# Kernel optimization log

Hardware: AMD Instinct MI355X
Metric: run time of the kernel (lower is better)

Reference implementation:

```python
import jax, jax.numpy as jnp
import numpy as np

K = 20
EPS = 1e-5
SLOPE = 0.2


def knn_idx(x, k):
    # x: (B, C, N) -> neighbor indices (B, N, k) by smallest squared distance
    xx = jnp.sum(x * x, axis=1)                      # (B, N)
    inner = jnp.einsum('bcn,bcm->bnm', x, x)         # (B, N, N)
    neg_dist = 2.0 * inner - xx[:, :, None] - xx[:, None, :]
    return jax.lax.top_k(neg_dist, k)[1]             # (B, N, k)


def bn_lrelu(y, g, b, axes):
    # training-mode BatchNorm (batch stats) + LeakyReLU(0.2); channel = last axis
    m = jnp.mean(y, axis=axes, keepdims=True)
    v = jnp.var(y, axis=axes, keepdims=True)
    y = (y - m) * jax.lax.rsqrt(v + EPS) * g + b
    return jnp.where(y > 0, y, SLOPE * y)


def edge_block(x, W, g, b, k):
    # x: (B, C, N); W: (out, 2C). Returns (B, N, out) = max over k neighbors.
    idx = knn_idx(x, k)                              # (B, N, k)
    xt = jnp.transpose(x, (0, 2, 1))                 # (B, N, C)
    feat = jax.vmap(lambda a, i: a[i])(xt, idx)      # (B, N, k, C) gather
    ctr = jnp.broadcast_to(xt[:, :, None, :], feat.shape)
    e = jnp.concatenate([feat - ctr, ctr], axis=-1)  # (B, N, k, 2C)
    y = jnp.einsum('bnkc,oc->bnko', e, W)            # 1x1 conv
    y = bn_lrelu(y, g, b, (0, 1, 2))
    return jnp.max(y, axis=2)                        # (B, N, out)


def setup_inputs() -> dict:
    key = jax.random.key(0)
    ks = jax.random.split(key, 7)
    feat_dims = [64, 64, 128, 256]
    in_dims = [2 * 3, 2 * 64, 2 * 64, 2 * 128]
    B, N = 8, 1024
    d = {'x': jax.random.normal(ks[0], (B, N, 3), dtype=jnp.float32)}
    for i, (ci, co) in enumerate(zip(in_dims, feat_dims)):
        d[f'W{i}'] = jax.random.normal(ks[i + 1], (co, ci), dtype=jnp.float32) * (1.0 / np.sqrt(ci))
        d[f'g{i}'] = jnp.ones((co,), dtype=jnp.float32)
        d[f'b{i}'] = jnp.zeros((co,), dtype=jnp.float32)
    fuse, emb = sum(feat_dims), 1024
    d['Wf'] = jax.random.normal(ks[5], (emb, fuse), dtype=jnp.float32) * (1.0 / np.sqrt(fuse))
    d['gf'] = jnp.ones((emb,), dtype=jnp.float32)
    d['bf'] = jnp.zeros((emb,), dtype=jnp.float32)
    return d


def reference(x, W0, g0, b0, W1, g1, b1, W2, g2, b2, W3, g3, b3, Wf, gf, bf):
    # x: (B, N, 3) -> (B, N, emb)
    h = jnp.transpose(x, (0, 2, 1))                  # (B, 3, N)
    states = []
    for (W, g, b) in [(W0, g0, b0), (W1, g1, b1), (W2, g2, b2), (W3, g3, b3)]:
        hn = edge_block(h, W, g, b, K)               # (B, N, out)
        states.append(hn)
        h = jnp.transpose(hn, (0, 2, 1))             # (B, out, N)
    fused = jnp.concatenate(states, axis=-1)         # (B, N, 512)
    y = jnp.einsum('bnc,oc->bno', fused, Wf)         # final 1x1 conv
    y = bn_lrelu(y, gf, bf, (0, 1))
    return y
```

## Files before the change

### kernel.cpp

```cpp
#include <hip/hip_runtime.h>
#include <math.h>

#define TILE 64
#define KC 16

typedef __attribute__((ext_vector_type(8))) short short8;
typedef __attribute__((ext_vector_type(4))) float float4v;
typedef const __attribute__((address_space(1))) void* gptr_t;
typedef __attribute__((address_space(3))) void* lptr_t;

#define OFF_DF    0ull
#define OFF_PT    0ull
#define OFF_YMAX  16777216ull
#define OFF_YMIN  25165824ull
#define OFF_YF    0ull
#define OFF_IDX   67108864ull
#define OFF_H     67764224ull
#define OFF_FUSB  76152832ull
#define OFF_WFB   84541440ull
#define OFF_XX    85590016ull
#define OFF_WCAT  85655552ull
#define OFF_STATS 85917696ull
#define OFF_COEF  85942272ull
#define OFF_HHI   85954560ull
#define OFF_HLO   88051712ull

__device__ __forceinline__ unsigned short f2bf(float f) {
  unsigned int u = __float_as_uint(f);
  unsigned int r = (u + 0x7fffu + ((u >> 16) & 1u)) >> 16;
  return (unsigned short)r;
}

__device__ __forceinline__ void gemm_tile_loop(
    const float* __restrict__ A, const float* __restrict__ Bw,
    int K, int lda, int ldb, int rowBase, int colBase,
    float acc[4][4], float* As, float* Bs)
{
  const int tid = threadIdx.x;
  const int tx = tid & 15, ty = tid >> 4;
  for (int k0 = 0; k0 < K; k0 += KC) {
    for (int l = 0; l < 4; ++l) {
      int flat = tid * 4 + l;
      int kk = flat & (KC - 1);
      int row = flat >> 4;
      int gk = k0 + kk;
      float av = 0.f, bv = 0.f;
      if (gk < K) {
        av = A[(size_t)(rowBase + row) * lda + gk];
        bv = Bw[(size_t)(colBase + row) * ldb + gk];
      }
      As[kk * TILE + row] = av;
      Bs[kk * TILE + row] = bv;
    }
    __syncthreads();
#pragma unroll
    for (int kk = 0; kk < KC; ++kk) {
      float a0[4], b0[4];
#pragma unroll
      for (int i = 0; i < 4; ++i) a0[i] = As[kk * TILE + ty * 4 + i];
#pragma unroll
      for (int j = 0; j < 4; ++j) b0[j] = Bs[kk * TILE + tx * 4 + j];
#pragma unroll
      for (int i = 0; i < 4; ++i)
#pragma unroll
        for (int j = 0; j < 4; ++j)
          acc[i][j] = fmaf(a0[i], b0[j], acc[i][j]);
    }
    __syncthreads();
  }
}

__global__ __launch_bounds__(256) void xxf_kernel(const float* __restrict__ H, int C,
                                                  float* __restrict__ xx) {
  int m = blockIdx.x * 256 + threadIdx.x;
  if (m < 8192) {
    float s = 0.f;
    for (int c = 0; c < C; ++c) { float h = H[(size_t)m * C + c]; s = fmaf(h, h, s); }
    xx[m] = s;
  }
}

__global__ __launch_bounds__(256) void split_bf16(const float* __restrict__ H, int C, int l2kp,
                                                  unsigned short* __restrict__ hi,
                                                  unsigned short* __restrict__ lo) {
  int i = blockIdx.x * 256 + threadIdx.x;
  int m = i >> l2kp;
  int c = i & ((1 << l2kp) - 1);
  unsigned short h = 0, l = 0;
  if (c < C) {
    float v = H[(size_t)m * C + c];
    h = f2bf(v);
    float hf = __uint_as_float((unsigned)h << 16);
    l = f2bf(v - hf);
  }
  hi[i] = h;
  lo[i] = l;
}

__global__ __launch_bounds__(256) void dist_mfma(const unsigned short* __restrict__ Hhi,
                                                 const unsigned short* __restrict__ Hlo,
                                                 const float* __restrict__ xx,
                                                 float* __restrict__ Df, int Kp) {
  __shared__ unsigned short Ash[128 * 32], Asl[128 * 32];
  __shared__ unsigned short Bsh[128 * 32], Bsl[128 * 32];
  const int tid = threadIdx.x;
  const int lane = tid & 63;
  const int w = tid >> 6;
  const int wm = w >> 1, wn = w & 1;
  const int bz = blockIdx.z;
  const int rowBase = bz * 1024 + blockIdx.y * 128;
  const int colBase = bz * 1024 + blockIdx.x * 128;
  const int quad = lane >> 4;
  const int l15 = lane & 15;

  float4v acc[4][4] = {};

  for (int k0 = 0; k0 < Kp; k0 += 32) {
#pragma unroll
    for (int q = 0; q < 2; ++q) {
      int ch = (w * 2 + q) * 64 + lane;
      int r = ch >> 2, cp = ch & 3;
      size_t offA = (size_t)(rowBase + r) * Kp + k0 + cp * 8;
      size_t offB = (size_t)(colBase + r) * Kp + k0 + cp * 8;
      int seg = (w * 2 + q) * 512;
      __builtin_amdgcn_global_load_lds((gptr_t)(Hhi + offA), (lptr_t)(Ash + seg), 16, 0, 0);
      __builtin_amdgcn_global_load_lds((gptr_t)(Hlo + offA), (lptr_t)(Asl + seg), 16, 0, 0);
      __builtin_amdgcn_global_load_lds((gptr_t)(Hhi + offB), (lptr_t)(Bsh + seg), 16, 0, 0);
      __builtin_amdgcn_global_load_lds((gptr_t)(Hlo + offB), (lptr_t)(Bsl + seg), 16, 0, 0);
    }
    __syncthreads();
    short8 ah[4], al[4], bh[4], bl[4];
#pragma unroll
    for (int mi = 0; mi < 4; ++mi) {
      int ro = (wm * 64 + mi * 16 + l15) * 32 + quad * 8;
      ah[mi] = *(const short8*)(Ash + ro);
      al[mi] = *(const short8*)(Asl + ro);
    }
#pragma unroll
    for (int ni = 0; ni < 4; ++ni) {
      int ro = (wn * 64 + ni * 16 + l15) * 32 + quad * 8;
      bh[ni] = *(const short8*)(Bsh + ro);
      bl[ni] = *(const short8*)(Bsl + ro);
    }
#pragma unroll
    for (int mi = 0; mi < 4; ++mi)
#pragma unroll
      for (int ni = 0; ni < 4; ++ni) {
        acc[mi][ni] = __builtin_amdgcn_mfma_f32_16x16x32_bf16(ah[mi], bh[ni], acc[mi][ni], 0, 0, 0);
        acc[mi][ni] = __builtin_amdgcn_mfma_f32_16x16x32_bf16(ah[mi], bl[ni], acc[mi][ni], 0, 0, 0);
        acc[mi][ni] = __builtin_amdgcn_mfma_f32_16x16x32_bf16(al[mi], bh[ni], acc[mi][ni], 0, 0, 0);
      }
    __syncthreads();
  }
#pragma unroll
  for (int mi = 0; mi < 4; ++mi)
#pragma unroll
    for (int ni = 0; ni < 4; ++ni)
#pragma unroll
      for (int r = 0; r < 4; ++r) {
        int gm = rowBase + wm * 64 + mi * 16 + quad * 4 + r;
        int gn = blockIdx.x * 128 + wn * 64 + ni * 16 + l15;
        float v = 2.0f * acc[mi][ni][r] - xx[gm] - xx[bz * 1024 + gn];
        Df[(size_t)gm * 1024 + gn] = v;
      }
}

template<int C>
__global__ __launch_bounds__(256) void topk_rerank(const float* __restrict__ Df,
                                                   const float* __restrict__ H,
                                                   int* __restrict__ idx) {
  __shared__ int    candLds[4][64];
  __shared__ double ndLds[4][64];
  __shared__ int    colLds[4][64];
  const int lane = threadIdx.x & 63;
  const int w = threadIdx.x >> 6;
  const int row = blockIdx.x * 4 + w;
  const int b = row >> 10;
  const float* drow = Df + (size_t)row * 1024;

  unsigned s[16];
#pragma unroll
  for (int q = 0; q < 4; ++q) {
    float4v v = *(const float4v*)(drow + 256 * q + 4 * lane);
#pragma unroll
    for (int r = 0; r < 4; ++r) {
      float f = (r == 0) ? v.x : (r == 1) ? v.y : (r == 2) ? v.z : v.w;
      unsigned u = __float_as_uint(f);
      s[q * 4 + r] = (u & 0x80000000u) ? ~u : (u | 0x80000000u);
    }
  }

  unsigned p = 0;
  for (int bit = 31; bit >= 0; --bit) {
    unsigned cand = p | (1u << bit);
    int c = 0;
#pragma unroll
    for (int t = 0; t < 16; ++t)
      c += __popcll(__ballot(s[t] > cand));
    if (c >= 32) {
      p = cand;
      if (c <= 64) break;
    }
  }

  const unsigned long long lt = (1ull << lane) - 1ull;
  int base = 0;
#pragma unroll
  for (int t = 0; t < 16; ++t) {
    unsigned long long m = __ballot(s[t] > p);
    if (s[t] > p) {
      int slot = base + (int)__popcll(m & lt);
      if (slot < 64) candLds[w][slot] = 256 * (t >> 2) + 4 * lane + (t & 3);
    }
    base += (int)__popcll(m);
  }
  int nsel = base > 64 ? 64 : base;

  double nd; int col;
  if (lane < nsel) {
    col = candLds[w][lane];
    const float* xi = H + (size_t)row * C;
    const float* xj = H + (size_t)(b * 1024 + col) * C;
    double ssum = 0.0;
    if (C == 3) {
#pragma unroll
      for (int c = 0; c < 3; ++c) {
        double d = (double)xi[c] - (double)xj[c];
        ssum = fma(d, d, ssum);
      }
    } else {
      for (int c = 0; c < C; c += 4) {
        float4v a = *(const float4v*)(xi + c);
        float4v bb = *(const float4v*)(xj + c);
        double d0 = (double)a.x - (double)bb.x;
        double d1 = (double)a.y - (double)bb.y;
        double d2 = (double)a.z - (double)bb.z;
        double d3 = (double)a.w - (double)bb.w;
        ssum = fma(d0, d0, ssum); ssum = fma(d1, d1, ssum);
        ssum = fma(d2, d2, ssum); ssum = fma(d3, d3, ssum);
      }
    }
    nd = -ssum;
  } else {
    nd = -INFINITY; col = 100000 + lane;
  }
  ndLds[w][lane] = nd;
  colLds[w][lane] = col;

  int rank = 0;
#pragma unroll 4
  for (int j = 0; j < 64; ++j) {
    double vj = ndLds[w][j];
    int cj = colLds[w][j];
    rank += (vj > nd || (vj == nd && cj < col)) ? 1 : 0;
  }
  if (rank < 20) idx[(size_t)row * 20 + rank] = col;
}

__global__ __launch_bounds__(256) void wcat_kernel(const float* __restrict__ W,
                                                   float* __restrict__ Wcat, int outc, int C) {
  int i = blockIdx.x * 256 + threadIdx.x;
  if (i < outc * C) {
    int o = i / C, c = i % C;
    float w1 = W[(size_t)o * 2 * C + c];
    float w2 = W[(size_t)o * 2 * C + C + c];
    Wcat[(size_t)o * C + c] = w1;
    Wcat[(size_t)(outc + o) * C + c] = w2 - w1;
  }
}

__global__ __launch_bounds__(256) void pt_gemm(const float* __restrict__ A,
                                               const float* __restrict__ Bw,
                                               float* __restrict__ Out, int K, int Nn) {
  __shared__ float As[KC * TILE], Bs[KC * TILE];
  int rowBase = blockIdx.y * 64, colBase = blockIdx.x * 64;
  float acc[4][4] = {};
  gemm_tile_loop(A, Bw, K, K, K, rowBase, colBase, acc, As, Bs);
  int tx = threadIdx.x & 15, ty = threadIdx.x >> 4;
#pragma unroll
  for (int i = 0; i < 4; ++i)
#pragma unroll
    for (int j = 0; j < 4; ++j)
      Out[(size_t)(rowBase + ty * 4 + i) * Nn + colBase + tx * 4 + j] = acc[i][j];
}

__global__ __launch_bounds__(256) void edge_reduce(const float* __restrict__ PT,
                                                   const int* __restrict__ idx,
                                                   float* __restrict__ ymax, float* __restrict__ ymin,
                                                   double* __restrict__ sum, double* __restrict__ sumsq,
                                                   int outc, int l2) {
  __shared__ int sidx[16 * 20];
  __shared__ float ssum[256], ssq[256];
  int tid = threadIdx.x;
  int base = blockIdx.x * 16;
  for (int i = tid; i < 320; i += 256) sidx[i] = idx[base * 20 + i];
  __syncthreads();
  int o = tid & (outc - 1);
  int rs = tid >> l2;
  int R = 256 >> l2;
  int twoc = 2 * outc;
  float ls = 0.f, lq = 0.f;
  for (int r = rs; r < 16; r += R) {
    int m = base + r;
    int boff = (m >> 10) << 10;
    float tv = PT[(size_t)m * twoc + outc + o];
    float vmax = -INFINITY, vmin = INFINITY;
#pragma unroll
    for (int k = 0; k < 20; ++k) {
      int nb = sidx[r * 20 + k];
      float p = PT[(size_t)(boff + nb) * twoc + o];
      float y = p + tv;
      vmax = fmaxf(vmax, y);
      vmin = fminf(vmin, y);
      ls += y;
      lq = fmaf(y, y, lq);
    }
    ymax[(size_t)m * outc + o] = vmax;
    ymin[(size_t)m * outc + o] = vmin;
  }
  ssum[tid] = ls; ssq[tid] = lq;
  __syncthreads();
  if (tid < outc) {
    float s = ssum[tid], q = ssq[tid];
    for (int rr = 1; rr < R; ++rr) { s += ssum[tid + rr * outc]; q += ssq[tid + rr * outc]; }
    atomicAdd(&sum[tid], (double)s);
    atomicAdd(&sumsq[tid], (double)q);
  }
}

__global__ __launch_bounds__(256) void coef_kernel(const double* __restrict__ sum,
                                                   const double* __restrict__ sumsq,
                                                   const float* __restrict__ g,
                                                   const float* __restrict__ b,
                                                   float* __restrict__ cA, float* __restrict__ cC,
                                                   int outc, double count) {
  int o = blockIdx.x * 256 + threadIdx.x;
  if (o < outc) {
    double mean = sum[o] / count;
    double var = sumsq[o] / count - mean * mean;
    double a = (double)g[o] / sqrt(var + 1e-5);
    cA[o] = (float)a;
    cC[o] = (float)((double)b[o] - mean * a);
  }
}

__global__ __launch_bounds__(256) void edge_epi(const float* __restrict__ ymax,
                                                const float* __restrict__ ymin,
                                                const float* __restrict__ cA, const float* __restrict__ cC,
                                                float* __restrict__ Hout, unsigned short* __restrict__ fusedb,
                                                int outc, int l2, int choff) {
  int i = blockIdx.x * 256 + threadIdx.x;
  int m = i >> l2;
  int o = i & (outc - 1);
  float a = cA[o], c = cC[o];
  float v = (a >= 0.f) ? ymax[i] : ymin[i];
  float y = fmaf(a, v, c);
  y = (y > 0.f) ? y : 0.2f * y;
  Hout[i] = y;
  fusedb[(size_t)m * 512 + choff + o] = f2bf(y);
}

__global__ __launch_bounds__(256) void cvt_bf16(const float* __restrict__ in,
                                                unsigned short* __restrict__ out, int n) {
  int i = blockIdx.x * 256 + threadIdx.x;
  if (i < n) out[i] = f2bf(in[i]);
}

__global__ __launch_bounds__(256) void final_gemm_mfma(const unsigned short* __restrict__ A,
                                                       const unsigned short* __restrict__ B,
                                                       float* __restrict__ C) {
  __shared__ unsigned short As[128 * 32];
  __shared__ unsigned short Bs[128 * 32];
  const int tid = threadIdx.x;
  const int lane = tid & 63;
  const int w = tid >> 6;
  const int wm = w >> 1, wn = w & 1;
  const int rowBase = blockIdx.y * 128;
  const int colBase = blockIdx.x * 128;
  const int quad = lane >> 4;
  const int l15 = lane & 15;

  float4v acc[4][4] = {};

  for (int k0 = 0; k0 < 512; k0 += 32) {
#pragma unroll
    for (int q = 0; q < 2; ++q) {
      int ch = (w * 2 + q) * 64 + lane;
      int r = ch >> 2, cp = ch & 3;
      const unsigned short* ga = A + (size_t)(rowBase + r) * 512 + k0 + cp * 8;
      const unsigned short* gb = B + (size_t)(colBase + r) * 512 + k0 + cp * 8;
      __builtin_amdgcn_global_load_lds((gptr_t)ga, (lptr_t)(As + (size_t)(w * 2 + q) * 512), 16, 0, 0);
      __builtin_amdgcn_global_load_lds((gptr_t)gb, (lptr_t)(Bs + (size_t)(w * 2 + q) * 512), 16, 0, 0);
    }
    __syncthreads();
    short8 af[4], bf[4];
#pragma unroll
    for (int mi = 0; mi < 4; ++mi)
      af[mi] = *(const short8*)(As + (wm * 64 + mi * 16 + l15) * 32 + quad * 8);
#pragma unroll
    for (int ni = 0; ni < 4; ++ni)
      bf[ni] = *(const short8*)(Bs + (wn * 64 + ni * 16 + l15) * 32 + quad * 8);
#pragma unroll
    for (int mi = 0; mi < 4; ++mi)
#pragma unroll
      for (int ni = 0; ni < 4; ++ni)
        acc[mi][ni] = __builtin_amdgcn_mfma_f32_16x16x32_bf16(af[mi], bf[ni], acc[mi][ni], 0, 0, 0);
    __syncthreads();
  }
#pragma unroll
  for (int mi = 0; mi < 4; ++mi)
#pragma unroll
    for (int ni = 0; ni < 4; ++ni)
#pragma unroll
      for (int r = 0; r < 4; ++r) {
        int gm = rowBase + wm * 64 + mi * 16 + quad * 4 + r;
        int gn = colBase + wn * 64 + ni * 16 + l15;
        C[(size_t)gm * 1024 + gn] = acc[mi][ni][r];
      }
}

__global__ __launch_bounds__(256) void col_stats(const float* __restrict__ yf,
                                                 double* __restrict__ sum, double* __restrict__ sumsq) {
  int col = blockIdx.x * 256 + threadIdx.x;
  int r0 = blockIdx.y * 128;
  float s = 0.f, q = 0.f;
  for (int r = 0; r < 128; ++r) {
    float v = yf[(size_t)(r0 + r) * 1024 + col];
    s += v;
    q = fmaf(v, v, q);
  }
  atomicAdd(&sum[col], (double)s);
  atomicAdd(&sumsq[col], (double)q);
}

__global__ __launch_bounds__(256) void final_epi(const float* __restrict__ yf,
                                                 const float* __restrict__ cA, const float* __restrict__ cC,
                                                 float* __restrict__ out) {
  int i = blockIdx.x * 256 + threadIdx.x;
  int o = i & 1023;
  float y = fmaf(cA[o], yf[i], cC[o]);
  out[i] = (y > 0.f) ? y : 0.2f * y;
}

extern "C" void kernel_launch(void* const* d_in, const int* in_sizes, int n_in,
                              void* d_out, int out_size, void* d_ws, size_t ws_size,
                              hipStream_t stream) {
  const float* x = (const float*)d_in[0];
  const float* W[4]  = {(const float*)d_in[1], (const float*)d_in[4], (const float*)d_in[7], (const float*)d_in[10]};
  const float* g[4]  = {(const float*)d_in[2], (const float*)d_in[5], (const float*)d_in[8], (const float*)d_in[11]};
  const float* bb[4] = {(const float*)d_in[3], (const float*)d_in[6], (const float*)d_in[9], (const float*)d_in[12]};
  const float* Wf  = (const float*)d_in[13];
  const float* gf  = (const float*)d_in[14];
  const float* bfp = (const float*)d_in[15];
  float* out = (float*)d_out;

  char* ws = (char*)d_ws;
  float*  Df    = (float*)(ws + OFF_DF);
  float*  PT    = (float*)(ws + OFF_PT);
  float*  ymax  = (float*)(ws + OFF_YMAX);
  float*  ymin  = (float*)(ws + OFF_YMIN);
  float*  yf    = (float*)(ws + OFF_YF);
  int*    idxb  = (int*)(ws + OFF_IDX);
  float*  Hbuf  = (float*)(ws + OFF_H);
  unsigned short* fusedb = (unsigned short*)(ws + OFF_FUSB);
  unsigned short* wfb    = (unsigned short*)(ws + OFF_WFB);
  float*  xxb   = (float*)(ws + OFF_XX);
  float*  wcat  = (float*)(ws + OFF_WCAT);
  double* stats = (double*)(ws + OFF_STATS);
  float*  coefb = (float*)(ws + OFF_COEF);
  unsigned short* hhi = (unsigned short*)(ws + OFF_HHI);
  unsigned short* hlo = (unsigned short*)(ws + OFF_HLO);

  hipMemsetAsync(stats, 0, 24576, stream);
  cvt_bf16<<<(524288 + 255) / 256, 256, 0, stream>>>(Wf, wfb, 524288);

  const int Cin[4]   = {3, 64, 64, 128};
  const int Cout[4]  = {64, 64, 128, 256};
  const int choff[4] = {0, 64, 128, 256};
  const float* Hin = x;
  size_t soff = 0, coff = 0;

  for (int i = 0; i < 4; ++i) {
    int C = Cin[i], oc = Cout[i];
    int l2 = (oc == 64) ? 6 : (oc == 128) ? 7 : 8;
    int Kp = (C == 3) ? 32 : C;
    int l2kp = (Kp == 32) ? 5 : (Kp == 64) ? 6 : 7;
    double* sum = stats + soff;  double* sumsq = sum + oc;  soff += 2 * (size_t)oc;
    float* cA = coefb + coff;    float* cC = cA + oc;       coff += 2 * (size_t)oc;

    xxf_kernel<<<32, 256, 0, stream>>>(Hin, C, xxb);
    split_bf16<<<(8192 << l2kp) / 256, 256, 0, stream>>>(Hin, C, l2kp, hhi, hlo);
    dist_mfma<<<dim3(8, 8, 8), 256, 0, stream>>>(hhi, hlo, xxb, Df, Kp);
    if (C == 3)       topk_rerank<3><<<2048, 256, 0, stream>>>(Df, Hin, idxb);
    else if (C == 64) topk_rerank<64><<<2048, 256, 0, stream>>>(Df, Hin, idxb);
    else              topk_rerank<128><<<2048, 256, 0, stream>>>(Df, Hin, idxb);
    wcat_kernel<<<(oc * C + 255) / 256, 256, 0, stream>>>(W[i], wcat, oc, C);
    pt_gemm<<<dim3(2 * oc / 64, 128), 256, 0, stream>>>(Hin, wcat, PT, C, 2 * oc);
    edge_reduce<<<512, 256, 0, stream>>>(PT, idxb, ymax, ymin, sum, sumsq, oc, l2);
    coef_kernel<<<1, 256, 0, stream>>>(sum, sumsq, g[i], bb[i], cA, cC, oc, 163840.0);
    edge_epi<<<(8192 * oc) / 256, 256, 0, stream>>>(ymax, ymin, cA, cC, Hbuf, fusedb, oc, l2, choff[i]);
    Hin = Hbuf;
  }

  double* sumF = stats + soff;  double* sumsqF = sumF + 1024;
  float* cAF = coefb + coff;    float* cCF = cAF + 1024;
  final_gemm_mfma<<<dim3(8, 64), 256, 0, stream>>>(fusedb, wfb, yf);
  col_stats<<<dim3(4, 64), 256, 0, stream>>>(yf, sumF, sumsqF);
  coef_kernel<<<4, 256, 0, stream>>>(sumF, sumsqF, gf, bfp, cAF, cCF, 1024, 8192.0);
  final_epi<<<8192 * 1024 / 256, 256, 0, stream>>>(yf, cAF, cCF, out);
}
```

Before: 524.9 us.

## Vectorize edge kernels and fuse final column stats into GEMM epilogue

Edge reduction, edge epilogue and final epilogue now handle four channels per thread with float4 loads and stores, so they issue fewer, wider memory transactions. The final GEMM accumulates per-column sum and sum-of-squares in its epilogue, reducing them through shared memory before the atomic adds, so the separate col_stats pass that re-read the 32MB output is removed. WCAT moves to a new workspace offset. In exchange, edge_reduce runs four times fewer threads per row, which lowers parallelism for the 64-channel layers.

Result: slower. 662.5 us (+26.2%).

```diff
diff --git a/kernel.cpp b/kernel.cpp
--- a/kernel.cpp
+++ b/kernel.cpp
@@ -6,6 +6,7 @@
 
 typedef __attribute__((ext_vector_type(8))) short short8;
 typedef __attribute__((ext_vector_type(4))) float float4v;
+typedef __attribute__((ext_vector_type(4))) unsigned short ushort4v;
 typedef const __attribute__((address_space(1))) void* gptr_t;
 typedef __attribute__((address_space(3))) void* lptr_t;
 
@@ -19,16 +20,19 @@
 #define OFF_FUSB  76152832ull
 #define OFF_WFB   84541440ull
 #define OFF_XX    85590016ull
-#define OFF_WCAT  85655552ull
 #define OFF_STATS 85917696ull
 #define OFF_COEF  85942272ull
 #define OFF_HHI   85954560ull
 #define OFF_HLO   88051712ull
+#define OFF_WCAT  90148864ull
 
 __device__ __forceinline__ unsigned short f2bf(float f) {
   unsigned int u = __float_as_uint(f);
   unsigned int r = (u + 0x7fffu + ((u >> 16) & 1u)) >> 16;
   return (unsigned short)r;
+}
+__device__ __forceinline__ float bf2f(unsigned short h) {
+  return __uint_as_float((unsigned)h << 16);
 }
 
 __device__ __forceinline__ void gemm_tile_loop(
@@ -90,8 +94,7 @@
   if (c < C) {
     float v = H[(size_t)m * C + c];
     h = f2bf(v);
-    float hf = __uint_as_float((unsigned)h << 16);
-    l = f2bf(v - hf);
+    l = f2bf(v - bf2f(h));
   }
   hi[i] = h;
   lo[i] = l;
@@ -184,8 +187,7 @@
     float4v v = *(const float4v*)(drow + 256 * q + 4 * lane);
 #pragma unroll
     for (int r = 0; r < 4; ++r) {
-      float f = (r == 0) ? v.x : (r == 1) ? v.y : (r == 2) ? v.z : v.w;
-      unsigned u = __float_as_uint(f);
+      unsigned u = __float_as_uint(v[r]);
       s[q * 4 + r] = (u & 0x80000000u) ? ~u : (u | 0x80000000u);
     }
   }
@@ -288,43 +290,51 @@
                                                    const int* __restrict__ idx,
                                                    float* __restrict__ ymax, float* __restrict__ ymin,
                                                    double* __restrict__ sum, double* __restrict__ sumsq,
-                                                   int outc, int l2) {
+                                                   int outc, int l2o4) {
   __shared__ int sidx[16 * 20];
-  __shared__ float ssum[256], ssq[256];
+  __shared__ float4v ssum[256], ssq[256];
   int tid = threadIdx.x;
   int base = blockIdx.x * 16;
   for (int i = tid; i < 320; i += 256) sidx[i] = idx[base * 20 + i];
   __syncthreads();
-  int o = tid & (outc - 1);
-  int rs = tid >> l2;
-  int R = 256 >> l2;
+  int tpp = outc >> 2;
+  int o4 = (tid & (tpp - 1)) << 2;
+  int rs = tid >> l2o4;
+  int R = 256 >> l2o4;
   int twoc = 2 * outc;
-  float ls = 0.f, lq = 0.f;
+  float4v ls = {0.f, 0.f, 0.f, 0.f}, lq = {0.f, 0.f, 0.f, 0.f};
   for (int r = rs; r < 16; r += R) {
     int m = base + r;
-    int boff = (m >> 10) << 10;
-    float tv = PT[(size_t)m * twoc + outc + o];
-    float vmax = -INFINITY, vmin = INFINITY;
+    int boff = m & ~1023;
+    float4v tv = *(const float4v*)(PT + (size_t)m * twoc + outc + o4);
+    float4v vmax = {-INFINITY, -INFINITY, -INFINITY, -INFINITY};
+    float4v vmin = {INFINITY, INFINITY, INFINITY, INFINITY};
 #pragma unroll
     for (int k = 0; k < 20; ++k) {
       int nb = sidx[r * 20 + k];
-      float p = PT[(size_t)(boff + nb) * twoc + o];
-      float y = p + tv;
-      vmax = fmaxf(vmax, y);
-      vmin = fminf(vmin, y);
+      float4v pv = *(const float4v*)(PT + (size_t)(boff + nb) * twoc + o4);
+      float4v y = pv + tv;
+#pragma unroll
+      for (int j = 0; j < 4; ++j) {
+        vmax[j] = fmaxf(vmax[j], y[j]);
+        vmin[j] = fminf(vmin[j], y[j]);
+      }
       ls += y;
-      lq = fmaf(y, y, lq);
-    }
-    ymax[(size_t)m * outc + o] = vmax;
-    ymin[(size_t)m * outc + o] = vmin;
+      lq += y * y;
+    }
+    *(float4v*)(ymax + (size_t)m * outc + o4) = vmax;
+    *(float4v*)(ymin + (size_t)m * outc + o4) = vmin;
   }
   ssum[tid] = ls; ssq[tid] = lq;
   __syncthreads();
-  if (tid < outc) {
-    float s = ssum[tid], q = ssq[tid];
-    for (int rr = 1; rr < R; ++rr) { s += ssum[tid + rr * outc]; q += ssq[tid + rr * outc]; }
-    atomicAdd(&sum[tid], (double)s);
-    atomicAdd(&sumsq[tid], (double)q);
+  if (tid < tpp) {
+    float4v s = ssum[tid], q = ssq[tid];
+    for (int rr = 1; rr < R; ++rr) { s += ssum[tid + rr * tpp]; q += ssq[tid + rr * tpp]; }
+#pragma unroll
+    for (int j = 0; j < 4; ++j) {
+      atomicAdd(&sum[(tid << 2) + j], (double)s[j]);
+      atomicAdd(&sumsq[(tid << 2) + j], (double)q[j]);
+    }
   }
 }
 
@@ -348,16 +358,27 @@
                                                 const float* __restrict__ ymin,
                                                 const float* __restrict__ cA, const float* __restrict__ cC,
                                                 float* __restrict__ Hout, unsigned short* __restrict__ fusedb,
-                                                int outc, int l2, int choff) {
-  int i = blockIdx.x * 256 + threadIdx.x;
-  int m = i >> l2;
-  int o = i & (outc - 1);
-  float a = cA[o], c = cC[o];
-  float v = (a >= 0.f) ? ymax[i] : ymin[i];
-  float y = fmaf(a, v, c);
-  y = (y > 0.f) ? y : 0.2f * y;
-  Hout[i] = y;
-  fusedb[(size_t)m * 512 + choff + o] = f2bf(y);
+                                                int outc, int l2o4, int choff) {
+  int i4 = blockIdx.x * 256 + threadIdx.x;
+  int tpp = outc >> 2;
+  int m = i4 >> l2o4;
+  int o4 = (i4 & (tpp - 1)) << 2;
+  float4v a = *(const float4v*)(cA + o4);
+  float4v c = *(const float4v*)(cC + o4);
+  float4v vx = *(const float4v*)(ymax + (size_t)i4 * 4);
+  float4v vn = *(const float4v*)(ymin + (size_t)i4 * 4);
+  float4v y;
+  ushort4v fb;
+#pragma unroll
+  for (int j = 0; j < 4; ++j) {
+    float v = (a[j] >= 0.f) ? vx[j] : vn[j];
+    float yy = fmaf(a[j], v, c[j]);
+    yy = (yy > 0.f) ? yy : 0.2f * yy;
+    y[j] = yy;
+    fb[j] = f2bf(yy);
+  }
+  *(float4v*)(Hout + (size_t)i4 * 4) = y;
+  *(ushort4v*)(fusedb + (size_t)m * 512 + choff + o4) = fb;
 }
 
 __global__ __launch_bounds__(256) void cvt_bf16(const float* __restrict__ in,
@@ -368,7 +389,9 @@
 
 __global__ __launch_bounds__(256) void final_gemm_mfma(const unsigned short* __restrict__ A,
                                                        const unsigned short* __restrict__ B,
-                                                       float* __restrict__ C) {
+                                                       float* __restrict__ C,
+                                                       double* __restrict__ sum,
+                                                       double* __restrict__ sumsq) {
   __shared__ unsigned short As[128 * 32];
   __shared__ unsigned short Bs[128 * 32];
   const int tid = threadIdx.x;
@@ -407,6 +430,7 @@
         acc[mi][ni] = __builtin_amdgcn_mfma_f32_16x16x32_bf16(af[mi], bf[ni], acc[mi][ni], 0, 0, 0);
     __syncthreads();
   }
+  float sc[4] = {0.f, 0.f, 0.f, 0.f}, qc[4] = {0.f, 0.f, 0.f, 0.f};
 #pragma unroll
   for (int mi = 0; mi < 4; ++mi)
 #pragma unroll
@@ -415,31 +439,45 @@
       for (int r = 0; r < 4; ++r) {
         int gm = rowBase + wm * 64 + mi * 16 + quad * 4 + r;
         int gn = colBase + wn * 64 + ni * 16 + l15;
-        C[(size_t)gm * 1024 + gn] = acc[mi][ni][r];
-      }
-}
-
-__global__ __launch_bounds__(256) void col_stats(const float* __restrict__ yf,
-                                                 double* __restrict__ sum, double* __restrict__ sumsq) {
-  int col = blockIdx.x * 256 + threadIdx.x;
-  int r0 = blockIdx.y * 128;
-  float s = 0.f, q = 0.f;
-  for (int r = 0; r < 128; ++r) {
-    float v = yf[(size_t)(r0 + r) * 1024 + col];
-    s += v;
-    q = fmaf(v, v, q);
-  }
-  atomicAdd(&sum[col], (double)s);
-  atomicAdd(&sumsq[col], (double)q);
+        float v = acc[mi][ni][r];
+        C[(size_t)gm * 1024 + gn] = v;
+        sc[ni] += v;
+        qc[ni] = fmaf(v, v, qc[ni]);
+      }
+  float* fs = (float*)As;
+  float* fq = (float*)Bs;
+#pragma unroll
+  for (int ni = 0; ni < 4; ++ni) {
+    int cl = wn * 64 + ni * 16 + l15;
+    int ct = wm * 4 + quad;
+    fs[cl * 8 + ct] = sc[ni];
+    fq[cl * 8 + ct] = qc[ni];
+  }
+  __syncthreads();
+  if (tid < 128) {
+    float s = 0.f, q = 0.f;
+#pragma unroll
+    for (int j = 0; j < 8; ++j) { s += fs[tid * 8 + j]; q += fq[tid * 8 + j]; }
+    atomicAdd(&sum[colBase + tid], (double)s);
+    atomicAdd(&sumsq[colBase + tid], (double)q);
+  }
 }
 
 __global__ __launch_bounds__(256) void final_epi(const float* __restrict__ yf,
                                                  const float* __restrict__ cA, const float* __restrict__ cC,
                                                  float* __restrict__ out) {
-  int i = blockIdx.x * 256 + threadIdx.x;
-  int o = i & 1023;
-  float y = fmaf(cA[o], yf[i], cC[o]);
-  out[i] = (y > 0.f) ? y : 0.2f * y;
+  int i4 = blockIdx.x * 256 + threadIdx.x;
+  int o4 = (i4 & 255) << 2;
+  float4v a = *(const float4v*)(cA + o4);
+  float4v c = *(const float4v*)(cC + o4);
+  float4v v = *(const float4v*)(yf + (size_t)i4 * 4);
+  float4v y;
+#pragma unroll
+  for (int j = 0; j < 4; ++j) {
+    float yy = fmaf(a[j], v[j], c[j]);
+    y[j] = (yy > 0.f) ? yy : 0.2f * yy;
+  }
+  *(float4v*)(out + (size_t)i4 * 4) = y;
 }
 
 extern "C" void kernel_launch(void* const* d_in, const int* in_sizes, int n_in,
@@ -465,11 +503,11 @@
   unsigned short* fusedb = (unsigned short*)(ws + OFF_FUSB);
   unsigned short* wfb    = (unsigned short*)(ws + OFF_WFB);
   float*  xxb   = (float*)(ws + OFF_XX);
-  float*  wcat  = (float*)(ws + OFF_WCAT);
   double* stats = (double*)(ws + OFF_STATS);
   float*  coefb = (float*)(ws + OFF_COEF);
   unsigned short* hhi = (unsigned short*)(ws + OFF_HHI);
   unsigned short* hlo = (unsigned short*)(ws + OFF_HLO);
+  float*  wcat  = (float*)(ws + OFF_WCAT);
 
   hipMemsetAsync(stats, 0, 24576, stream);
   cvt_bf16<<<(524288 + 255) / 256, 256, 0, stream>>>(Wf, wfb, 524288);
@@ -482,7 +520,7 @@
 
   for (int i = 0; i < 4; ++i) {
     int C = Cin[i], oc = Cout[i];
-    int l2 = (oc == 64) ? 6 : (oc == 128) ? 7 : 8;
+    int l2o4 = (oc == 64) ? 4 : (oc == 128) ? 5 : 6;
     int Kp = (C == 3) ? 32 : C;
     int l2kp = (Kp == 32) ? 5 : (Kp == 64) ? 6 : 7;
     double* sum = stats + soff;  double* sumsq = sum + oc;  soff += 2 * (size_t)oc;
@@ -496,16 +534,15 @@
     else              topk_rerank<128><<<2048, 256, 0, stream>>>(Df, Hin, idxb);
     wcat_kernel<<<(oc * C + 255) / 256, 256, 0, stream>>>(W[i], wcat, oc, C);
     pt_gemm<<<dim3(2 * oc / 64, 128), 256, 0, stream>>>(Hin, wcat, PT, C, 2 * oc);
-    edge_reduce<<<512, 256, 0, stream>>>(PT, idxb, ymax, ymin, sum, sumsq, oc, l2);
+    edge_reduce<<<512, 256, 0, stream>>>(PT, idxb, ymax, ymin, sum, sumsq, oc, l2o4);
     coef_kernel<<<1, 256, 0, stream>>>(sum, sumsq, g[i], bb[i], cA, cC, oc, 163840.0);
-    edge_epi<<<(8192 * oc) / 256, 256, 0, stream>>>(ymax, ymin, cA, cC, Hbuf, fusedb, oc, l2, choff[i]);
+    edge_epi<<<(8192 * oc / 4) / 256, 256, 0, stream>>>(ymax, ymin, cA, cC, Hbuf, fusedb, oc, l2o4, choff[i]);
     Hin = Hbuf;
   }
 
   double* sumF = stats + soff;  double* sumsqF = sumF + 1024;
   float* cAF = coefb + coff;    float* cCF = cAF + 1024;
-  final_gemm_mfma<<<dim3(8, 64), 256, 0, stream>>>(fusedb, wfb, yf);
-  col_stats<<<dim3(4, 64), 256, 0, stream>>>(yf, sumF, sumsqF);
+  final_gemm_mfma<<<dim3(8, 64), 256, 0, stream>>>(fusedb, wfb, yf, sumF, sumsqF);
   coef_kernel<<<4, 256, 0, stream>>>(sumF, sumsqF, gf, bfp, cAF, cCF, 1024, 8192.0);
-  final_epi<<<8192 * 1024 / 256, 256, 0, stream>>>(yf, cAF, cCF, out);
-}
+  final_epi<<<8192 * 1024 / 4 / 256, 256, 0, stream>>>(yf, cAF, cCF, out);
+}
```
